# Kernel tuning notes

Measured on AMD Instinct MI355X. Metric: run time of the kernel, lower is better.

The kernel has to match this reference:

```python
import jax, jax.numpy as jnp
import numpy as np

HEADS = 8
DIM_HEAD = 64
SCALE = DIM_HEAD ** -0.5


def setup_inputs() -> dict:
    key = jax.random.key(0)
    k1, k2, k3 = jax.random.split(key, 3)
    b, dim, n = 4, 256, 2048
    hidden = HEADS * DIM_HEAD  # 512
    x = jax.random.normal(k1, (b, dim, n), dtype=jnp.float32)
    # Conv1d kernel-size-1 weights are pointwise linear maps over channels.
    w_qkv = jax.random.normal(k2, (3 * hidden, dim), dtype=jnp.float32) * (dim ** -0.5)
    w_out = jax.random.normal(k3, (dim, hidden), dtype=jnp.float32) * (hidden ** -0.5)
    b_out = jnp.zeros((dim,), dtype=jnp.float32)
    return {"x": x, "w_qkv": w_qkv, "w_out": w_out, "b_out": b_out}


def reference(x, w_qkv, w_out, b_out):
    b, dim, n = x.shape
    hidden = w_out.shape[1]
    # pointwise conv1d == channel matmul: [3h, dim] x [b, dim, n] -> [b, 3h, n]
    qkv = jnp.einsum('oi,bin->bon', w_qkv, x)
    q, k, v = jnp.split(qkv, 3, axis=1)
    # b (h c) n -> b h c n
    reshape = lambda t: t.reshape(b, HEADS, DIM_HEAD, n)
    q, k, v = reshape(q) * SCALE, reshape(k), reshape(v)
    sim = jnp.einsum('bhdi,bhdj->bhij', q, k)          # [b, h, n, n]
    attn = jax.nn.softmax(sim, axis=-1)
    out = jnp.einsum('bhij,bhdj->bhid', attn, v)        # [b, h, n, d]
    # b h n d -> b (h d) n
    out = out.transpose(0, 1, 3, 2).reshape(b, hidden, n)
    return jnp.einsum('oi,bin->bon', w_out, out) + b_out[None, :, None]
```

## Files before the change

kernel.cpp:

```cpp
#include <hip/hip_runtime.h>
#include <stdint.h>

#define SEQ  2048
#define DIMC 256
#define HID  512
#define NH   8
#define DH   64

typedef __attribute__((ext_vector_type(8))) short bf16x8;
typedef __attribute__((ext_vector_type(4))) float f32x4;
typedef __attribute__((ext_vector_type(16))) float f32x16;
typedef __attribute__((ext_vector_type(2))) unsigned uint2v;
typedef __attribute__((address_space(1))) const uint32_t guint_t;
typedef __attribute__((address_space(3))) uint32_t luint_t;

__device__ __forceinline__ void gld16(const void* g, void* l) {
  __builtin_amdgcn_global_load_lds((guint_t*)g, (luint_t*)l, 16, 0, 0);
}

__device__ __forceinline__ unsigned short f2bf(float f) {
  union { float f; uint32_t u; } v; v.f = f;
  return (unsigned short)((v.u + 0x7FFFu + ((v.u >> 16) & 1u)) >> 16);
}

__device__ __forceinline__ uint32_t fbits(float f) {
  union { float f; uint32_t u; } v; v.f = f; return v.u;
}

__device__ __forceinline__ uint32_t pku(uint32_t u0, uint32_t u1) {
  return __builtin_amdgcn_perm(u1 + 0x8000u, u0 + 0x8000u, 0x07060302u);
}

__device__ __forceinline__ void swap32(uint32_t& a, uint32_t& b) {
#if __has_builtin(__builtin_amdgcn_permlane32_swap)
  uint2v r = __builtin_amdgcn_permlane32_swap(a, b, false, false);
  a = r[0]; b = r[1];
#else
  uint32_t aw = __shfl_xor(a, 32);
  uint32_t bw = __shfl_xor(b, 32);
  bool lo = (threadIdx.x & 32) == 0;
  uint32_t an = lo ? a : bw;
  uint32_t bn = lo ? aw : b;
  a = an; b = bn;
#endif
}

__global__ __launch_bounds__(256) void prep_kernel(
    const float* __restrict__ x, const float* __restrict__ wqkv,
    const float* __restrict__ wout,
    unsigned short* __restrict__ wqkv_b, unsigned short* __restrict__ wout_b,
    unsigned short* __restrict__ xT) {
  __shared__ float tile[64][65];
  int blk = blockIdx.x;
  int t = threadIdx.x;
  if (blk < 384) {
    int idx = blk * 1024 + t * 4;
    float4 v = *(const float4*)(wqkv + idx);
    float s = ((idx >> 8) < HID) ? 0.18033688011112042f : 1.0f;
    ushort4 o;
    o.x = f2bf(v.x * s); o.y = f2bf(v.y * s);
    o.z = f2bf(v.z * s); o.w = f2bf(v.w * s);
    *(ushort4*)(wqkv_b + idx) = o;
    return;
  }
  if (blk < 512) {
    int idx = (blk - 384) * 1024 + t * 4;
    float4 v = *(const float4*)(wout + idx);
    ushort4 o;
    o.x = f2bf(v.x); o.y = f2bf(v.y); o.z = f2bf(v.z); o.w = f2bf(v.w);
    *(ushort4*)(wout_b + idx) = o;
    return;
  }
  int tid = blk - 512;
  int b  = tid >> 7;
  int r  = tid & 127;
  int i0 = (r >> 5) * 64;
  int n0 = (r & 31) * 64;
  const float* xb = x + (size_t)b * DIMC * SEQ;
  int tn = t & 15, ti = t >> 4;
#pragma unroll
  for (int j = 0; j < 4; j++) {
    int il = ti + j * 16;
    float4 v = *(const float4*)(xb + (size_t)(i0 + il) * SEQ + n0 + tn * 4);
    tile[il][tn*4+0] = v.x; tile[il][tn*4+1] = v.y;
    tile[il][tn*4+2] = v.z; tile[il][tn*4+3] = v.w;
  }
  __syncthreads();
  unsigned short* xTb = xT + (size_t)b * SEQ * DIMC;
#pragma unroll
  for (int j = 0; j < 4; j++) {
    int nl = ti + j * 16;
    int i4 = tn * 4;
    uint2 pk;
    pk.x = (uint32_t)f2bf(tile[i4+0][nl]) | ((uint32_t)f2bf(tile[i4+1][nl]) << 16);
    pk.y = (uint32_t)f2bf(tile[i4+2][nl]) | ((uint32_t)f2bf(tile[i4+3][nl]) << 16);
    *(uint2*)(xTb + (size_t)(n0 + nl) * DIMC + i0 + i4) = pk;
  }
}

__global__ __launch_bounds__(256, 2) void qkv_gemm(
    const unsigned short* __restrict__ wq, const unsigned short* __restrict__ xT,
    unsigned short* __restrict__ Qs, unsigned short* __restrict__ Ks,
    unsigned short* __restrict__ Vt) {
  __shared__ unsigned short lds[17408];
  unsigned short* la = lds;
  unsigned short* lb = lds + 8192;
  int o0 = blockIdx.x * 128;
  int n0 = blockIdx.y * 128;
  int b  = blockIdx.z;
  int t  = threadIdx.x;
  int wv = t >> 6, l = t & 63, l15 = l & 15, q = l >> 4;
  int wm = (wv & 1) * 64, wn = (wv >> 1) * 64;
  f32x4 acc[4][4];
#pragma unroll
  for (int i = 0; i < 4; i++)
#pragma unroll
    for (int j = 0; j < 4; j++) acc[i][j] = (f32x4){0.f, 0.f, 0.f, 0.f};
  const unsigned short* Ag = wq + (size_t)o0 * DIMC;
  const unsigned short* Bg = xT + ((size_t)b * SEQ + n0) * DIMC;
  int lrow8 = l >> 3, lcol = l & 7;
  for (int kk = 0; kk < 4; kk++) {
    int k0 = kk * 64;
    __syncthreads();
#pragma unroll
    for (int c0 = 0; c0 < 4; c0++) {
      int c = wv * 4 + c0;
      int row = c * 8 + lrow8;
      int sg = lcol ^ (row & 7);
      gld16(Ag + (size_t)row * DIMC + k0 + sg * 8, la + c * 512);
      gld16(Bg + (size_t)row * DIMC + k0 + sg * 8, lb + c * 512);
    }
    __syncthreads();
#pragma unroll
    for (int kh = 0; kh < 2; kh++) {
      bf16x8 af[4], bfr[4];
#pragma unroll
      for (int mt = 0; mt < 4; mt++) {
        int row = wm + mt*16 + l15;
        af[mt] = *(const bf16x8*)(la + row*64 + ((kh*4 + q) ^ (row & 7)) * 8);
      }
#pragma unroll
      for (int nt = 0; nt < 4; nt++) {
        int row = wn + nt*16 + l15;
        bfr[nt] = *(const bf16x8*)(lb + row*64 + ((kh*4 + q) ^ (row & 7)) * 8);
      }
#pragma unroll
      for (int mt = 0; mt < 4; mt++)
#pragma unroll
        for (int nt = 0; nt < 4; nt++)
          acc[mt][nt] = __builtin_amdgcn_mfma_f32_16x16x32_bf16(af[mt], bfr[nt], acc[mt][nt], 0, 0, 0);
    }
  }
  __syncthreads();
  int seg3 = o0 >> 9;
  int h0   = (o0 & 511) >> 6;
  if (seg3 == 2) {
#pragma unroll
    for (int mt = 0; mt < 4; mt++)
#pragma unroll
      for (int nt = 0; nt < 4; nt++)
#pragma unroll
        for (int r = 0; r < 4; r++) {
          int ol = wm + mt * 16 + q * 4 + r;
          int h = h0 + (ol >> 6), d = ol & 63;
          int n = n0 + wn + nt * 16 + l15;
          Vt[(((size_t)b * NH + h) * DH + d) * SEQ + n] = f2bf(acc[mt][nt][r]);
        }
  } else {
    unsigned short* dst = (seg3 == 0) ? Qs : Ks;
#pragma unroll
    for (int mt = 0; mt < 4; mt++)
#pragma unroll
      for (int nt = 0; nt < 4; nt++)
#pragma unroll
        for (int r = 0; r < 4; r++) {
          int ol = wm + mt * 16 + q * 4 + r;
          int nn = wn + nt * 16 + l15;
          lds[nn * 136 + ol] = f2bf(acc[mt][nt][r]);
        }
    __syncthreads();
#pragma unroll
    for (int i = 0; i < 8; i++) {
      int idx = i * 256 + t;
      int nn  = idx >> 4;
      int olb = (idx & 15) * 8;
      uint4 v = *(const uint4*)(lds + nn * 136 + olb);
      int h = h0 + (olb >> 6), d = olb & 63;
      *(uint4*)(dst + (((size_t)b * NH + h) * SEQ + n0 + nn) * DH + d) = v;
    }
  }
}

__global__ __launch_bounds__(256, 2) void attn_kernel(
    const unsigned short* __restrict__ Qs, const unsigned short* __restrict__ Ks,
    const unsigned short* __restrict__ Vt, unsigned short* __restrict__ AO) {
  __shared__ unsigned short KV[16384];
  __shared__ float Lc[256];
  int n0 = blockIdx.x * 128;
  int bh = blockIdx.y;
  int b = bh >> 3, h = bh & 7;
  int t = threadIdx.x;
  int w = t >> 6, l = t & 63, l31 = l & 31, lh = l >> 5, l7 = l & 7;
  int cg = w >> 1, qg = w & 1;
  const unsigned short* Qg = Qs + ((size_t)bh * SEQ + n0 + qg * 64) * DH;
  bf16x8 qb[2][4];
#pragma unroll
  for (int qt = 0; qt < 2; qt++)
#pragma unroll
    for (int kc = 0; kc < 4; kc++)
      qb[qt][kc] = *(const bf16x8*)(Qg + (qt*32 + l31) * DH + kc*16 + lh*8);
  f32x16 oacc[2][2];
  float lrowp[2] = {0.f, 0.f};
#pragma unroll
  for (int qt = 0; qt < 2; qt++)
#pragma unroll
    for (int dt = 0; dt < 2; dt++)
#pragma unroll
      for (int r = 0; r < 16; r++) oacc[qt][dt][r] = 0.f;
  const unsigned short* Kst = KV + cg * 4096;
  const unsigned short* Vst = KV + 8192 + cg * 4096;
  for (int it = 0; it < 16; it++) {
    int jb = it * 64;
    __syncthreads();
    if (w < 2) {
      const unsigned short* src = Ks + ((size_t)bh * SEQ + w * 1024 + jb) * DH;
      unsigned short* dst = (unsigned short*)KV + w * 4096;
#pragma unroll
      for (int g = 0; g < 8; g++) {
        int kr = g * 8 + (l >> 3);
        gld16(src + (size_t)kr * DH + (l7 ^ (kr & 7)) * 8, dst + g * 512);
      }
    } else {
      const unsigned short* src = Vt + (size_t)bh * DH * SEQ + (w - 2) * 1024 + jb;
      unsigned short* dst = (unsigned short*)KV + 8192 + (w - 2) * 4096;
#pragma unroll
      for (int g = 0; g < 8; g++) {
        int dr = g * 8 + (l >> 3);
        gld16(src + (size_t)dr * SEQ + (l7 ^ (dr & 7)) * 8, dst + g * 512);
      }
    }
    __syncthreads();
#pragma unroll
    for (int kb = 0; kb < 64; kb += 32) {
      f32x16 st[2];
#pragma unroll
      for (int qt = 0; qt < 2; qt++)
#pragma unroll
        for (int r = 0; r < 16; r++) st[qt][r] = 0.f;
#pragma unroll
      for (int kc = 0; kc < 4; kc++) {
        bf16x8 kf = *(const bf16x8*)(Kst + (kb + l31) * 64 + (((kc*2 + lh) ^ l7)) * 8);
        st[0] = __builtin_amdgcn_mfma_f32_32x32x16_bf16(kf, qb[0][kc], st[0], 0, 0, 0);
        st[1] = __builtin_amdgcn_mfma_f32_32x32x16_bf16(kf, qb[1][kc], st[1], 0, 0, 0);
      }
      bf16x8 vf[2][2];
#pragma unroll
      for (int kc2 = 0; kc2 < 2; kc2++)
#pragma unroll
        for (int dt = 0; dt < 2; dt++)
          vf[kc2][dt] = *(const bf16x8*)(Vst + (dt*32 + l31) * 64 +
                                         ((((kb >> 3) + kc2*2 + lh) ^ l7)) * 8);
#pragma unroll
      for (int qt = 0; qt < 2; qt++) {
        float p[16];
        float s0 = 0.f;
#pragma unroll
        for (int r = 0; r < 16; r++) { p[r] = __builtin_amdgcn_exp2f(st[qt][r]); s0 += p[r]; }
        lrowp[qt] += s0;
        bf16x8 af[2];
#pragma unroll
        for (int hf = 0; hf < 2; hf++) {
          uint32_t xs[4], ys[4];
#pragma unroll
          for (int j = 0; j < 4; j++) {
            xs[j] = fbits(p[hf*8 + j]);
            ys[j] = fbits(p[hf*8 + 4 + j]);
            swap32(xs[j], ys[j]);
          }
          uint32_t d0 = pku(xs[0], xs[1]);
          uint32_t d1 = pku(xs[2], xs[3]);
          uint32_t d2 = pku(ys[0], ys[1]);
          uint32_t d3 = pku(ys[2], ys[3]);
          union { uint32_t u[4]; bf16x8 v; } cv;
          cv.u[0] = d0; cv.u[1] = d1; cv.u[2] = d2; cv.u[3] = d3;
          af[hf] = cv.v;
        }
#pragma unroll
        for (int kc2 = 0; kc2 < 2; kc2++)
#pragma unroll
          for (int dt = 0; dt < 2; dt++)
            oacc[qt][dt] = __builtin_amdgcn_mfma_f32_32x32x16_bf16(af[kc2], vf[kc2][dt], oacc[qt][dt], 0, 0, 0);
      }
    }
  }
#pragma unroll
  for (int qt = 0; qt < 2; qt++) {
    float v = lrowp[qt];
    v += __shfl_xor(v, 32);
    if (l < 32) Lc[cg * 128 + qg * 64 + qt * 32 + l31] = v;
  }
  __syncthreads();
  float* Oc = (float*)KV;
  if (cg == 1) {
#pragma unroll
    for (int qt = 0; qt < 2; qt++)
#pragma unroll
      for (int dt = 0; dt < 2; dt++)
#pragma unroll
        for (int r = 0; r < 16; r++) {
          int qrow = qg*64 + qt*32 + (r & 3) + 8*(r >> 2) + 4*lh;
          Oc[qrow * 64 + dt*32 + l31] = oacc[qt][dt][r];
        }
  }
  __syncthreads();
  if (cg == 0) {
    unsigned short* AOb = AO + (size_t)b * SEQ * HID + h * DH;
#pragma unroll
    for (int qt = 0; qt < 2; qt++)
#pragma unroll
      for (int r = 0; r < 16; r++) {
        int qrow = qg*64 + qt*32 + (r & 3) + 8*(r >> 2) + 4*lh;
        float inv = __builtin_amdgcn_rcpf(Lc[qrow] + Lc[128 + qrow]);
        int n = n0 + qrow;
#pragma unroll
        for (int dt = 0; dt < 2; dt++) {
          float val = (oacc[qt][dt][r] + Oc[qrow * 64 + dt*32 + l31]) * inv;
          AOb[(size_t)n * HID + dt*32 + l31] = f2bf(val);
        }
      }
  }
}

__global__ __launch_bounds__(256, 2) void out_gemm(
    const unsigned short* __restrict__ wo, const unsigned short* __restrict__ AO,
    const float* __restrict__ bias, float* __restrict__ out) {
  __shared__ unsigned short la[64 * 64];
  __shared__ unsigned short lb[128 * 64];
  int o0 = blockIdx.x * 64;
  int n0 = blockIdx.y * 128;
  int b  = blockIdx.z;
  int t  = threadIdx.x;
  int wv = t >> 6, l = t & 63, l15 = l & 15, q = l >> 4;
  int wm = (wv & 1) * 32, wn = (wv >> 1) * 64;
  f32x4 acc[2][4];
#pragma unroll
  for (int i = 0; i < 2; i++)
#pragma unroll
    for (int j = 0; j < 4; j++) acc[i][j] = (f32x4){0.f,0.f,0.f,0.f};
  const unsigned short* Ag = wo + (size_t)o0 * HID;
  const unsigned short* Bg = AO + ((size_t)b * SEQ + n0) * HID;
  int lrow8 = l >> 3, lcol = l & 7;
  for (int kk = 0; kk < 8; kk++) {
    int k0 = kk * 64;
    __syncthreads();
#pragma unroll
    for (int c0 = 0; c0 < 2; c0++) {
      int c = wv * 2 + c0;
      int row = c * 8 + lrow8;
      int sg = lcol ^ (row & 7);
      gld16(Ag + (size_t)row * HID + k0 + sg * 8, la + c * 512);
    }
#pragma unroll
    for (int c0 = 0; c0 < 4; c0++) {
      int c = wv * 4 + c0;
      int row = c * 8 + lrow8;
      int sg = lcol ^ (row & 7);
      gld16(Bg + (size_t)row * HID + k0 + sg * 8, lb + c * 512);
    }
    __syncthreads();
#pragma unroll
    for (int kh = 0; kh < 2; kh++) {
      bf16x8 af[2], bfr[4];
#pragma unroll
      for (int mt = 0; mt < 2; mt++) {
        int row = wm + mt*16 + l15;
        af[mt] = *(const bf16x8*)(la + row*64 + ((kh*4 + q) ^ (row & 7)) * 8);
      }
#pragma unroll
      for (int nt = 0; nt < 4; nt++) {
        int row = wn + nt*16 + l15;
        bfr[nt] = *(const bf16x8*)(lb + row*64 + ((kh*4 + q) ^ (row & 7)) * 8);
      }
#pragma unroll
      for (int mt = 0; mt < 2; mt++)
#pragma unroll
        for (int nt = 0; nt < 4; nt++)
          acc[mt][nt] = __builtin_amdgcn_mfma_f32_16x16x32_bf16(af[mt], bfr[nt], acc[mt][nt], 0,0,0);
    }
  }
#pragma unroll
  for (int mt = 0; mt < 2; mt++)
#pragma unroll
    for (int nt = 0; nt < 4; nt++)
#pragma unroll
      for (int r = 0; r < 4; r++) {
        int o2 = o0 + wm + mt*16 + q*4 + r;
        int n  = n0 + wn + nt*16 + l15;
        out[((size_t)b * DIMC + o2) * SEQ + n] = acc[mt][nt][r] + bias[o2];
      }
}

extern "C" void kernel_launch(void* const* d_in, const int* in_sizes, int n_in,
                              void* d_out, int out_size, void* d_ws, size_t ws_size,
                              hipStream_t stream) {
  const float* x    = (const float*)d_in[0];
  const float* wqkv = (const float*)d_in[1];
  const float* wout = (const float*)d_in[2];
  const float* bout = (const float*)d_in[3];
  float* out = (float*)d_out;
  char* ws = (char*)d_ws;
  unsigned short* wqkv_b = (unsigned short*)(ws);
  unsigned short* wout_b = (unsigned short*)(ws + 786432);
  unsigned short* xT     = (unsigned short*)(ws + 1048576);
  unsigned short* Qs     = (unsigned short*)(ws + 5242880);
  unsigned short* Ks     = (unsigned short*)(ws + 13631488);
  unsigned short* Vt     = (unsigned short*)(ws + 22020096);
  unsigned short* AO     = (unsigned short*)(ws + 30408704);
  prep_kernel<<<1024, 256, 0, stream>>>(x, wqkv, wout, wqkv_b, wout_b, xT);
  qkv_gemm<<<dim3(12, 16, 4), 256, 0, stream>>>(wqkv_b, xT, Qs, Ks, Vt);
  attn_kernel<<<dim3(16, 32), 256, 0, stream>>>(Qs, Ks, Vt, AO);
  out_gemm<<<dim3(4, 16, 4), 256, 0, stream>>>(wout_b, AO, bout, out);
}
```

Before: 134.7 us.

## Double-buffer LDS tiles with async global-to-LDS prefetch in all three kernels

Converts the qkv GEMM, attention, and output GEMM loops to double-buffered LDS staging. The next tile is issued via global_load_lds before the current tile is computed, and partial vmcnt waits with raw barriers replace the full __syncthreads pairs. This is meant to hide global load latency behind MFMA work. In exchange, LDS use per block doubles (64KB in qkv/attn), which may reduce occupancy, and correctness depends on the hand-counted vmcnt values.

```diff
diff --git a/kernel.cpp b/kernel.cpp
--- a/kernel.cpp
+++ b/kernel.cpp
@@ -17,6 +17,13 @@
 __device__ __forceinline__ void gld16(const void* g, void* l) {
   __builtin_amdgcn_global_load_lds((guint_t*)g, (luint_t*)l, 16, 0, 0);
 }
+
+__device__ __forceinline__ void barrier_raw() {
+  asm volatile("" ::: "memory");
+  __builtin_amdgcn_s_barrier();
+  asm volatile("" ::: "memory");
+}
+#define WAITVM(n) asm volatile("s_waitcnt vmcnt(" #n ")" ::: "memory")
 
 __device__ __forceinline__ unsigned short f2bf(float f) {
   union { float f; uint32_t u; } v; v.f = f;
@@ -102,9 +109,7 @@
     const unsigned short* __restrict__ wq, const unsigned short* __restrict__ xT,
     unsigned short* __restrict__ Qs, unsigned short* __restrict__ Ks,
     unsigned short* __restrict__ Vt) {
-  __shared__ unsigned short lds[17408];
-  unsigned short* la = lds;
-  unsigned short* lb = lds + 8192;
+  __shared__ unsigned short lds[32768];
   int o0 = blockIdx.x * 128;
   int n0 = blockIdx.y * 128;
   int b  = blockIdx.z;
@@ -119,9 +124,11 @@
   const unsigned short* Ag = wq + (size_t)o0 * DIMC;
   const unsigned short* Bg = xT + ((size_t)b * SEQ + n0) * DIMC;
   int lrow8 = l >> 3, lcol = l & 7;
-  for (int kk = 0; kk < 4; kk++) {
+
+  auto stage = [&](int kk, int buf) {
+    unsigned short* la = lds + (buf << 14);
+    unsigned short* lb = la + 8192;
     int k0 = kk * 64;
-    __syncthreads();
 #pragma unroll
     for (int c0 = 0; c0 < 4; c0++) {
       int c = wv * 4 + c0;
@@ -130,7 +137,16 @@
       gld16(Ag + (size_t)row * DIMC + k0 + sg * 8, la + c * 512);
       gld16(Bg + (size_t)row * DIMC + k0 + sg * 8, lb + c * 512);
     }
-    __syncthreads();
+  };
+
+  stage(0, 0);
+  for (int kk = 0; kk < 4; kk++) {
+    int cur = kk & 1;
+    if (kk < 3) { stage(kk + 1, cur ^ 1); WAITVM(8); }
+    else        { WAITVM(0); }
+    barrier_raw();
+    unsigned short* la = lds + (cur << 14);
+    unsigned short* lb = la + 8192;
 #pragma unroll
     for (int kh = 0; kh < 2; kh++) {
       bf16x8 af[4], bfr[4];
@@ -150,8 +166,8 @@
         for (int nt = 0; nt < 4; nt++)
           acc[mt][nt] = __builtin_amdgcn_mfma_f32_16x16x32_bf16(af[mt], bfr[nt], acc[mt][nt], 0, 0, 0);
     }
-  }
-  __syncthreads();
+    barrier_raw();
+  }
   int seg3 = o0 >> 9;
   int h0   = (o0 & 511) >> 6;
   if (seg3 == 2) {
@@ -194,7 +210,7 @@
 __global__ __launch_bounds__(256, 2) void attn_kernel(
     const unsigned short* __restrict__ Qs, const unsigned short* __restrict__ Ks,
     const unsigned short* __restrict__ Vt, unsigned short* __restrict__ AO) {
-  __shared__ unsigned short KV[16384];
+  __shared__ unsigned short KVs[32768];
   __shared__ float Lc[256];
   int n0 = blockIdx.x * 128;
   int bh = blockIdx.y;
@@ -217,14 +233,13 @@
     for (int dt = 0; dt < 2; dt++)
 #pragma unroll
       for (int r = 0; r < 16; r++) oacc[qt][dt][r] = 0.f;
-  const unsigned short* Kst = KV + cg * 4096;
-  const unsigned short* Vst = KV + 8192 + cg * 4096;
-  for (int it = 0; it < 16; it++) {
-    int jb = it * 64;
-    __syncthreads();
+
+  auto stage = [&](int it2, int buf) {
+    int jb = it2 * 64;
+    unsigned short* base = KVs + (buf << 14);
     if (w < 2) {
       const unsigned short* src = Ks + ((size_t)bh * SEQ + w * 1024 + jb) * DH;
-      unsigned short* dst = (unsigned short*)KV + w * 4096;
+      unsigned short* dst = base + w * 4096;
 #pragma unroll
       for (int g = 0; g < 8; g++) {
         int kr = g * 8 + (l >> 3);
@@ -232,14 +247,23 @@
       }
     } else {
       const unsigned short* src = Vt + (size_t)bh * DH * SEQ + (w - 2) * 1024 + jb;
-      unsigned short* dst = (unsigned short*)KV + 8192 + (w - 2) * 4096;
+      unsigned short* dst = base + 8192 + (w - 2) * 4096;
 #pragma unroll
       for (int g = 0; g < 8; g++) {
         int dr = g * 8 + (l >> 3);
         gld16(src + (size_t)dr * SEQ + (l7 ^ (dr & 7)) * 8, dst + g * 512);
       }
     }
-    __syncthreads();
+  };
+
+  stage(0, 0);
+  for (int it = 0; it < 16; it++) {
+    int cur = it & 1;
+    if (it < 15) { stage(it + 1, cur ^ 1); WAITVM(8); }
+    else         { WAITVM(0); }
+    barrier_raw();
+    const unsigned short* Kst = KVs + (cur << 14) + cg * 4096;
+    const unsigned short* Vst = KVs + (cur << 14) + 8192 + cg * 4096;
 #pragma unroll
     for (int kb = 0; kb < 64; kb += 32) {
       f32x16 st[2];
@@ -292,6 +316,7 @@
             oacc[qt][dt] = __builtin_amdgcn_mfma_f32_32x32x16_bf16(af[kc2], vf[kc2][dt], oacc[qt][dt], 0, 0, 0);
       }
     }
+    barrier_raw();
   }
 #pragma unroll
   for (int qt = 0; qt < 2; qt++) {
@@ -300,7 +325,7 @@
     if (l < 32) Lc[cg * 128 + qg * 64 + qt * 32 + l31] = v;
   }
   __syncthreads();
-  float* Oc = (float*)KV;
+  float* Oc = (float*)KVs;
   if (cg == 1) {
 #pragma unroll
     for (int qt = 0; qt < 2; qt++)
@@ -334,8 +359,7 @@
 __global__ __launch_bounds__(256, 2) void out_gemm(
     const unsigned short* __restrict__ wo, const unsigned short* __restrict__ AO,
     const float* __restrict__ bias, float* __restrict__ out) {
-  __shared__ unsigned short la[64 * 64];
-  __shared__ unsigned short lb[128 * 64];
+  __shared__ unsigned short lds[24576];
   int o0 = blockIdx.x * 64;
   int n0 = blockIdx.y * 128;
   int b  = blockIdx.z;
@@ -350,9 +374,11 @@
   const unsigned short* Ag = wo + (size_t)o0 * HID;
   const unsigned short* Bg = AO + ((size_t)b * SEQ + n0) * HID;
   int lrow8 = l >> 3, lcol = l & 7;
-  for (int kk = 0; kk < 8; kk++) {
+
+  auto stage = [&](int kk, int buf) {
+    unsigned short* la = lds + buf * 12288;
+    unsigned short* lb = la + 4096;
     int k0 = kk * 64;
-    __syncthreads();
 #pragma unroll
     for (int c0 = 0; c0 < 2; c0++) {
       int c = wv * 2 + c0;
@@ -367,7 +393,16 @@
       int sg = lcol ^ (row & 7);
       gld16(Bg + (size_t)row * HID + k0 + sg * 8, lb + c * 512);
     }
-    __syncthreads();
+  };
+
+  stage(0, 0);
+  for (int kk = 0; kk < 8; kk++) {
+    int cur = kk & 1;
+    if (kk < 7) { stage(kk + 1, cur ^ 1); WAITVM(6); }
+    else        { WAITVM(0); }
+    barrier_raw();
+    unsigned short* la = lds + cur * 12288;
+    unsigned short* lb = la + 4096;
 #pragma unroll
     for (int kh = 0; kh < 2; kh++) {
       bf16x8 af[2], bfr[4];
@@ -387,6 +422,7 @@
         for (int nt = 0; nt < 4; nt++)
           acc[mt][nt] = __builtin_amdgcn_mfma_f32_16x16x32_bf16(af[mt], bfr[nt], acc[mt][nt], 0,0,0);
     }
+    barrier_raw();
   }
 #pragma unroll
   for (int mt = 0; mt < 2; mt++)
```

New measurement: 129.4 us. 1.04x faster.
